# Performance work log

Hardware: AMD Instinct MI355X
Metric: run time of the kernel (lower is better)

The kernel has to match this reference:

```python
import jax, jax.numpy as jnp
import numpy as np

N, E, C = 50000, 600000, 128
BN_EPS = 1e-5
NORM_EPS = 1e-12


def _edgeconv(x, src, dst, wa, ba, g, be, rm, rv, wb, bb):
    # PyG EdgeConv: message = MLP(concat(x_i, x_j - x_i)); aggr='add' at target i
    x_i = x[dst]                      # [E, C] target features
    x_j = x[src]                      # [E, C] source features
    m = jnp.concatenate([x_i, x_j - x_i], axis=-1)   # [E, 2C]
    m = jax.nn.relu(m @ wa.T + ba)                   # Linear(2C->C) + ReLU
    m = (m - rm) * (g * jax.lax.rsqrt(rv + BN_EPS)) + be  # BatchNorm1d (eval)
    m = m @ wb.T + bb                                # Linear(C->C)
    return jax.ops.segment_sum(m, dst, num_segments=x.shape[0])  # [N, C]


def _lin(k, fan_in, shape):
    bound = 1.0 / np.sqrt(fan_in)
    return jax.random.uniform(k, shape, jnp.float32, -bound, bound)


def setup_inputs() -> dict:
    key = jax.random.key(0)
    ks = jax.random.split(key, 16)
    inp = {
        "x": jax.random.normal(ks[0], (N, C), jnp.float32),
        "edge_index": jax.random.randint(ks[1], (2, E), 0, N, jnp.int64),
    }
    # layer 1 params
    inp["w1a"] = _lin(ks[2], 2 * C, (C, 2 * C)); inp["b1a"] = _lin(ks[3], 2 * C, (C,))
    inp["g1"] = jnp.ones((C,), jnp.float32) + 0.1 * jax.random.normal(ks[4], (C,))
    inp["be1"] = 0.1 * jax.random.normal(ks[5], (C,))
    inp["rm1"] = 0.1 * jax.random.normal(ks[6], (C,))
    inp["rv1"] = 0.5 + jax.random.uniform(ks[7], (C,))
    inp["w1b"] = _lin(ks[8], C, (C, C)); inp["b1b"] = _lin(ks[9], C, (C,))
    # layer 2 params
    inp["w2a"] = _lin(ks[10], 2 * C, (C, 2 * C)); inp["b2a"] = _lin(ks[11], 2 * C, (C,))
    inp["g2"] = jnp.ones((C,), jnp.float32) + 0.1 * jax.random.normal(ks[12], (C,))
    inp["be2"] = 0.1 * jax.random.normal(ks[13], (C,))
    inp["rm2"] = 0.1 * jax.random.normal(ks[14], (C,))
    inp["rv2"] = 0.5 + jax.random.uniform(ks[15], (C,))
    k2 = jax.random.split(ks[15], 2)
    inp["w2b"] = _lin(k2[0], C, (C, C)); inp["b2b"] = _lin(k2[1], C, (C,))
    return inp


def reference(x, edge_index, w1a, b1a, g1, be1, rm1, rv1, w1b, b1b,
              w2a, b2a, g2, be2, rm2, rv2, w2b, b2b):
    src, dst = edge_index[0], edge_index[1]
    # layer 1 (all but last): conv -> relu -> L2 normalize -> dropout(eval=identity)
    h = _edgeconv(x, src, dst, w1a, b1a, g1, be1, rm1, rv1, w1b, b1b)
    h = jax.nn.relu(h)
    h = h / jnp.maximum(jnp.linalg.norm(h, axis=-1, keepdims=True), NORM_EPS)
    # last layer: conv only
    return _edgeconv(h, src, dst, w2a, b2a, g2, be2, rm2, rv2, w2b, b2b)
```

## Files before the change

kernel.cpp:

```cpp
#include <hip/hip_runtime.h>

#define CCH 128
#define WPAD 136
typedef unsigned short ushort;
typedef __attribute__((ext_vector_type(8))) short bf16x8_t;
typedef __attribute__((ext_vector_type(4))) float f32x4;

union ABu { bf16x8_t v; ushort u[8]; uint4 q; };

__device__ __forceinline__ ushort f2b(float f) {
  union { float f; unsigned u; } v{f};
  unsigned r = v.u + 0x7fffu + ((v.u >> 16) & 1u);
  return (ushort)(r >> 16);
}
__device__ __forceinline__ float b2f(ushort s) {
  union { unsigned u; float f; } v{(unsigned)s << 16};
  return v.f;
}

__global__ void k_detect(const unsigned int* __restrict__ eiw, int* __restrict__ flags) {
  __shared__ int cz;
  int t = threadIdx.x;
  if (t == 0) cz = 0;
  __syncthreads();
  if (eiw[2 * t + 1] != 0u) atomicAdd(&cz, 1);
  __syncthreads();
  if (t == 0) flags[1] = (cz == 0) ? 1 : 0;
}

__device__ __forceinline__ int ldidx(const void* ei, size_t i, bool i64) {
  return i64 ? (int)((const long long*)ei)[i] : ((const int*)ei)[i];
}

__global__ void k_hist(const void* __restrict__ ei, int* __restrict__ deg, int E,
                       const int* __restrict__ flags) {
  bool i64 = flags[1] != 0;
  int e = blockIdx.x * 256 + threadIdx.x;
  if (e < E) atomicAdd(&deg[ldidx(ei, (size_t)E + e, i64)], 1);
}

__global__ void k_scan1(const int* __restrict__ deg, int* __restrict__ bsum, int n) {
  __shared__ int s[256];
  int t = threadIdx.x, i = blockIdx.x * 256 + t;
  s[t] = (i < n) ? deg[i] : 0;
  __syncthreads();
  for (int off = 128; off > 0; off >>= 1) {
    if (t < off) s[t] += s[t + off];
    __syncthreads();
  }
  if (t == 0) bsum[blockIdx.x] = s[0];
}

__global__ void k_scan2(const int* __restrict__ bsum, int* __restrict__ boff, int nb) {
  __shared__ int s[256];
  int t = threadIdx.x;
  int v = (t < nb) ? bsum[t] : 0;
  s[t] = v; __syncthreads();
  for (int off = 1; off < 256; off <<= 1) {
    int tv = (t >= off) ? s[t - off] : 0;
    __syncthreads();
    s[t] += tv;
    __syncthreads();
  }
  if (t < nb) boff[t] = s[t] - v;
}

__global__ void k_scan3(const int* __restrict__ deg, const int* __restrict__ boff,
                        int* __restrict__ rowptr, int n, int Etot) {
  __shared__ int s[256];
  int t = threadIdx.x, i = blockIdx.x * 256 + t;
  int v = (i < n) ? deg[i] : 0;
  s[t] = v; __syncthreads();
  for (int off = 1; off < 256; off <<= 1) {
    int tv = (t >= off) ? s[t - off] : 0;
    __syncthreads();
    s[t] += tv;
    __syncthreads();
  }
  if (i < n) rowptr[i] = boff[blockIdx.x] + s[t] - v;
  if (i == 0) rowptr[n] = Etot;
}

__global__ void k_scatter(const void* __restrict__ ei, const int* __restrict__ rowptr,
                          int* __restrict__ cnt, int* __restrict__ esrc, int E,
                          const int* __restrict__ flags) {
  bool i64 = flags[1] != 0;
  int e = blockIdx.x * 256 + threadIdx.x;
  if (e < E) {
    int d = ldidx(ei, (size_t)E + e, i64);
    int s = ldidx(ei, (size_t)e, i64);
    int pos = rowptr[d] + atomicAdd(&cnt[d], 1);
    esrc[pos] = s;
  }
}

__global__ void k_wconv(const float* __restrict__ wa, const float* __restrict__ wb,
                        ushort* __restrict__ Wcat, ushort* __restrict__ Wbb) {
  int i = blockIdx.x * 256 + threadIdx.x;
  if (i < 32768) {
    int c = i >> 7, k = i & 127;
    float v = (c < 128) ? wa[c * 256 + k] - wa[c * 256 + 128 + k]
                        : wa[(c - 128) * 256 + 128 + k];
    Wcat[i] = f2b(v);
  }
  if (i < 16384) Wbb[i] = f2b(wb[i]);
}

template <int EPI, typename TIN>
__global__ __launch_bounds__(256) void k_gemm(const TIN* __restrict__ X,
                                              const ushort* __restrict__ W,
                                              const float* __restrict__ bias,
                                              const int* __restrict__ deg,
                                              void* __restrict__ Y1,
                                              ushort* __restrict__ Y2, int nN) {
  constexpr int WN = (EPI == 0) ? 16 : 8;
  __shared__ ushort wlds[WN * 16 * WPAD];
  const int t = threadIdx.x;
  const int wave = t >> 6, lane = t & 63;
  const int ln = lane & 15, quad = lane >> 4;

  for (int i = t; i < WN * 256; i += 256) {
    int row = i >> 4, ch = i & 15;
    *(uint4*)&wlds[row * WPAD + ch * 8] = *(const uint4*)&W[row * CCH + ch * 8];
  }
  __syncthreads();

  const int rowb0 = blockIdx.x * 128 + wave * 32;
  const int rowb1 = rowb0 + 16;
  const int ar0 = rowb0 + ln, ar1 = rowb1 + ln;

  ABu a0[4], a1[4];
#pragma unroll
  for (int kk = 0; kk < 4; ++kk) {
    if constexpr (sizeof(TIN) == 4) {
      auto ldc = [&](int r, ABu& d) {
        if (r < nN) {
          const float* xp = (const float*)X + (size_t)r * CCH + kk * 32 + quad * 8;
          float4 f0 = *(const float4*)xp;
          float4 f1 = *(const float4*)(xp + 4);
          d.u[0] = f2b(f0.x); d.u[1] = f2b(f0.y); d.u[2] = f2b(f0.z); d.u[3] = f2b(f0.w);
          d.u[4] = f2b(f1.x); d.u[5] = f2b(f1.y); d.u[6] = f2b(f1.z); d.u[7] = f2b(f1.w);
        } else d.q = make_uint4(0, 0, 0, 0);
      };
      ldc(ar0, a0[kk]); ldc(ar1, a1[kk]);
    } else {
      a0[kk].q = (ar0 < nN) ? *(const uint4*)((const ushort*)X + (size_t)ar0 * CCH + kk * 32 + quad * 8)
                            : make_uint4(0, 0, 0, 0);
      a1[kk].q = (ar1 < nN) ? *(const uint4*)((const ushort*)X + (size_t)ar1 * CCH + kk * 32 + quad * 8)
                            : make_uint4(0, 0, 0, 0);
    }
  }

  f32x4 acc0[WN], acc1[WN];
#pragma unroll
  for (int s = 0; s < WN; ++s) {
    acc0[s] = (f32x4){0.f, 0.f, 0.f, 0.f};
    acc1[s] = (f32x4){0.f, 0.f, 0.f, 0.f};
  }

#pragma unroll
  for (int s = 0; s < WN; ++s) {
#pragma unroll
    for (int kk = 0; kk < 4; ++kk) {
      ABu b;
      b.q = *(const uint4*)&wlds[(s * 16 + ln) * WPAD + kk * 32 + quad * 8];
      acc0[s] = __builtin_amdgcn_mfma_f32_16x16x32_bf16(a0[kk].v, b.v, acc0[s], 0, 0, 0);
      acc1[s] = __builtin_amdgcn_mfma_f32_16x16x32_bf16(a1[kk].v, b.v, acc1[s], 0, 0, 0);
    }
  }

  if constexpr (EPI == 0) {
    ushort* A1 = (ushort*)Y1;
#pragma unroll
    for (int s = 0; s < 16; ++s) {
      int col = s * 16 + ln;
      float bv = (s < 8) ? bias[col] : 0.f;
#pragma unroll
      for (int r = 0; r < 4; ++r) {
        int row0 = rowb0 + quad * 4 + r, row1 = rowb1 + quad * 4 + r;
        if (row0 < nN) {
          if (s < 8) A1[(size_t)row0 * CCH + col] = f2b(acc0[s][r] + bv);
          else       Y2[(size_t)row0 * CCH + (col - 128)] = f2b(acc0[s][r]);
        }
        if (row1 < nN) {
          if (s < 8) A1[(size_t)row1 * CCH + col] = f2b(acc1[s][r] + bv);
          else       Y2[(size_t)row1 * CCH + (col - 128)] = f2b(acc1[s][r]);
        }
      }
    }
  } else if constexpr (EPI == 1) {
    ushort* H = (ushort*)Y1;
    float biasv[8];
#pragma unroll
    for (int s = 0; s < 8; ++s) biasv[s] = bias[s * 16 + ln];
    auto epi = [&](f32x4* acc, int rowb) {
#pragma unroll
      for (int r = 0; r < 4; ++r) {
        int row = rowb + quad * 4 + r;
        float dn = (row < nN) ? (float)deg[row] : 0.f;
        float vals[8];
        float ss = 0.f;
#pragma unroll
        for (int s = 0; s < 8; ++s) {
          float v = fmaxf(acc[s][r] + dn * biasv[s], 0.f);
          vals[s] = v;
          ss += v * v;
        }
        ss += __shfl_xor(ss, 1, 64);
        ss += __shfl_xor(ss, 2, 64);
        ss += __shfl_xor(ss, 4, 64);
        ss += __shfl_xor(ss, 8, 64);
        float inv = 1.0f / fmaxf(sqrtf(ss), 1e-12f);
        if (row < nN) {
#pragma unroll
          for (int s = 0; s < 8; ++s)
            H[(size_t)row * CCH + s * 16 + ln] = f2b(vals[s] * inv);
        }
      }
    };
    epi(acc0, rowb0); epi(acc1, rowb1);
  } else {
    float* OUT = (float*)Y1;
    float biasv[8];
#pragma unroll
    for (int s = 0; s < 8; ++s) biasv[s] = bias[s * 16 + ln];
    auto epi = [&](f32x4* acc, int rowb) {
#pragma unroll
      for (int r = 0; r < 4; ++r) {
        int row = rowb + quad * 4 + r;
        if (row >= nN) continue;
        float dn = (float)deg[row];
#pragma unroll
        for (int s = 0; s < 8; ++s)
          OUT[(size_t)row * CCH + s * 16 + ln] = acc[s][r] + dn * biasv[s];
      }
    };
    epi(acc0, rowb0); epi(acc1, rowb1);
  }
}

__global__ __launch_bounds__(256) void k_aggr(const ushort* __restrict__ A1,
                                              const ushort* __restrict__ A2,
                                              const int* __restrict__ rowptr,
                                              const int* __restrict__ esrc,
                                              const float* __restrict__ g,
                                              const float* __restrict__ be,
                                              const float* __restrict__ rm,
                                              const float* __restrict__ rv,
                                              ushort* __restrict__ M, int nNodes) {
  int node = blockIdx.x * 4 + (threadIdx.x >> 6);
  if (node >= nNodes) return;
  int lane = threadIdx.x & 63;
  int q = lane >> 4;
  int c = (lane & 15) * 8;

  uint4 aq = *(const uint4*)&A1[(size_t)node * CCH + c];
  float a[8] = {b2f((ushort)aq.x), b2f((ushort)(aq.x >> 16)),
                b2f((ushort)aq.y), b2f((ushort)(aq.y >> 16)),
                b2f((ushort)aq.z), b2f((ushort)(aq.z >> 16)),
                b2f((ushort)aq.w), b2f((ushort)(aq.w >> 16))};
  int r0 = rowptr[node], r1 = rowptr[node + 1];
  float s[8] = {0.f, 0.f, 0.f, 0.f, 0.f, 0.f, 0.f, 0.f};

  int e = r0 + q;
  for (; e + 4 < r1; e += 8) {
    int sA = esrc[e], sB = esrc[e + 4];
    uint4 wA = *(const uint4*)&A2[(size_t)sA * CCH + c];
    uint4 wB = *(const uint4*)&A2[(size_t)sB * CCH + c];
    const unsigned* pA = (const unsigned*)&wA;
    const unsigned* pB = (const unsigned*)&wB;
#pragma unroll
    for (int j = 0; j < 4; ++j) {
      s[2*j]   += fmaxf(a[2*j]   + b2f((ushort)pA[j]), 0.f);
      s[2*j+1] += fmaxf(a[2*j+1] + b2f((ushort)(pA[j] >> 16)), 0.f);
      s[2*j]   += fmaxf(a[2*j]   + b2f((ushort)pB[j]), 0.f);
      s[2*j+1] += fmaxf(a[2*j+1] + b2f((ushort)(pB[j] >> 16)), 0.f);
    }
  }
  for (; e < r1; e += 4) {
    int sA = esrc[e];
    uint4 wA = *(const uint4*)&A2[(size_t)sA * CCH + c];
    const unsigned* pA = (const unsigned*)&wA;
#pragma unroll
    for (int j = 0; j < 4; ++j) {
      s[2*j]   += fmaxf(a[2*j]   + b2f((ushort)pA[j]), 0.f);
      s[2*j+1] += fmaxf(a[2*j+1] + b2f((ushort)(pA[j] >> 16)), 0.f);
    }
  }
#pragma unroll
  for (int j = 0; j < 8; ++j) {
    s[j] += __shfl_xor(s[j], 16, 64);
    s[j] += __shfl_xor(s[j], 32, 64);
  }

  if (q == 0) {
    float dn = (float)(r1 - r0);
    unsigned p[4];
#pragma unroll
    for (int j = 0; j < 4; ++j) {
      float sc0 = g[c + 2*j]     * rsqrtf(rv[c + 2*j]     + 1e-5f);
      float sc1 = g[c + 2*j + 1] * rsqrtf(rv[c + 2*j + 1] + 1e-5f);
      float o0 = sc0 * s[2*j]     + dn * (be[c + 2*j]     - rm[c + 2*j]     * sc0);
      float o1 = sc1 * s[2*j + 1] + dn * (be[c + 2*j + 1] - rm[c + 2*j + 1] * sc1);
      p[j] = (unsigned)f2b(o0) | ((unsigned)f2b(o1) << 16);
    }
    *(uint4*)&M[(size_t)node * CCH + c] = make_uint4(p[0], p[1], p[2], p[3]);
  }
}

extern "C" void kernel_launch(void* const* d_in, const int* in_sizes, int n_in,
                              void* d_out, int out_size, void* d_ws, size_t ws_size,
                              hipStream_t stream) {
  const float* x   = (const float*)d_in[0];
  const void*  ei  = d_in[1];
  const float* w1a = (const float*)d_in[2];
  const float* b1a = (const float*)d_in[3];
  const float* g1  = (const float*)d_in[4];
  const float* be1 = (const float*)d_in[5];
  const float* rm1 = (const float*)d_in[6];
  const float* rv1 = (const float*)d_in[7];
  const float* w1b = (const float*)d_in[8];
  const float* b1b = (const float*)d_in[9];
  const float* w2a = (const float*)d_in[10];
  const float* b2a = (const float*)d_in[11];
  const float* g2  = (const float*)d_in[12];
  const float* be2 = (const float*)d_in[13];
  const float* rm2 = (const float*)d_in[14];
  const float* rv2 = (const float*)d_in[15];
  const float* w2b = (const float*)d_in[16];
  const float* b2b = (const float*)d_in[17];

  const int N = in_sizes[0] / CCH;
  const int E = in_sizes[1] / 2;
  const size_t NC = (size_t)N * CCH;

  int* flags  = (int*)d_ws;
  int* deg    = flags + 4;
  int* cnt    = deg + N;
  int* rowptr = cnt + N;
  int* bsum   = rowptr + N + 1;
  int* boff   = bsum + 256;
  int* esrc   = boff + 256;
  uintptr_t pw = ((uintptr_t)(esrc + E) + 63) & ~(uintptr_t)63;
  ushort* Wcat1 = (ushort*)pw;
  ushort* Wcat2 = Wcat1 + 32768;
  ushort* Wb1   = Wcat2 + 32768;
  ushort* Wb2   = Wb1 + 16384;
  uintptr_t pb = ((uintptr_t)(Wb2 + 16384) + 63) & ~(uintptr_t)63;
  ushort* B0 = (ushort*)pb;
  ushort* B1 = B0 + NC;
  ushort* MB = B1 + NC;
  ushort* HB = MB + NC;

  const int gE = (E + 255) / 256;
  const int gS = (N + 255) / 256;
  const int gG = (N + 127) / 128;
  const int gA = (N + 3) / 4;

  k_detect<<<1, 256, 0, stream>>>((const unsigned int*)ei, flags);
  hipMemsetAsync(deg, 0, sizeof(int) * 2 * (size_t)N, stream);
  k_wconv<<<128, 256, 0, stream>>>(w1a, w1b, Wcat1, Wb1);
  k_wconv<<<128, 256, 0, stream>>>(w2a, w2b, Wcat2, Wb2);
  k_hist<<<gE, 256, 0, stream>>>(ei, deg, E, flags);
  k_scan1<<<gS, 256, 0, stream>>>(deg, bsum, N);
  k_scan2<<<1, 256, 0, stream>>>(bsum, boff, gS);
  k_scan3<<<gS, 256, 0, stream>>>(deg, boff, rowptr, N, E);
  k_scatter<<<gE, 256, 0, stream>>>(ei, rowptr, cnt, esrc, E, flags);

  k_gemm<0, float><<<gG, 256, 0, stream>>>(x, Wcat1, b1a, nullptr, B0, B1, N);
  k_aggr<<<gA, 256, 0, stream>>>(B0, B1, rowptr, esrc, g1, be1, rm1, rv1, MB, N);
  k_gemm<1, ushort><<<gG, 256, 0, stream>>>(MB, Wb1, b1b, deg, HB, nullptr, N);
  k_gemm<0, ushort><<<gG, 256, 0, stream>>>(HB, Wcat2, b2a, nullptr, B0, B1, N);
  k_aggr<<<gA, 256, 0, stream>>>(B0, B1, rowptr, esrc, g2, be2, rm2, rv2, MB, N);
  k_gemm<2, ushort><<<gG, 256, 0, stream>>>(MB, Wb2, b2b, deg, d_out, nullptr, N);
}
```

Before: 313.4 us.

## Fuse setup kernels and shrink GEMM tiles with a column-split grid

```diff
diff --git a/kernel.cpp b/kernel.cpp
--- a/kernel.cpp
+++ b/kernel.cpp
@@ -18,18 +18,42 @@
   return v.f;
 }
 
-__global__ void k_detect(const unsigned int* __restrict__ eiw, int* __restrict__ flags) {
-  __shared__ int cz;
-  int t = threadIdx.x;
-  if (t == 0) cz = 0;
-  __syncthreads();
-  if (eiw[2 * t + 1] != 0u) atomicAdd(&cz, 1);
-  __syncthreads();
-  if (t == 0) flags[1] = (cz == 0) ? 1 : 0;
-}
-
 __device__ __forceinline__ int ldidx(const void* ei, size_t i, bool i64) {
   return i64 ? (int)((const long long*)ei)[i] : ((const int*)ei)[i];
+}
+
+__global__ void k_init(const unsigned int* __restrict__ eiw, int* __restrict__ flags,
+                       int* __restrict__ degcnt, int n2,
+                       const float* __restrict__ w1a, const float* __restrict__ w1b,
+                       const float* __restrict__ w2a, const float* __restrict__ w2b,
+                       ushort* __restrict__ Wcat1, ushort* __restrict__ Wb1,
+                       ushort* __restrict__ Wcat2, ushort* __restrict__ Wb2) {
+  int b = blockIdx.x, t = threadIdx.x;
+  int gid = b * 256 + t;
+  if (gid < n2) degcnt[gid] = 0;
+
+  if (b < 128) {
+    int i = gid;
+    int c = i >> 7, k = i & 127;
+    float v = (c < 128) ? w1a[c * 256 + k] - w1a[c * 256 + 128 + k]
+                        : w1a[(c - 128) * 256 + 128 + k];
+    Wcat1[i] = f2b(v);
+    if (i < 16384) Wb1[i] = f2b(w1b[i]);
+  } else if (b < 256) {
+    int i = gid - 32768;
+    int c = i >> 7, k = i & 127;
+    float v = (c < 128) ? w2a[c * 256 + k] - w2a[c * 256 + 128 + k]
+                        : w2a[(c - 128) * 256 + 128 + k];
+    Wcat2[i] = f2b(v);
+    if (i < 16384) Wb2[i] = f2b(w2b[i]);
+  } else if (b == 256) {
+    __shared__ int cz;
+    if (t == 0) cz = 0;
+    __syncthreads();
+    if (eiw[2 * t + 1] != 0u) atomicAdd(&cz, 1);
+    __syncthreads();
+    if (t == 0) flags[1] = (cz == 0) ? 1 : 0;
+  }
 }
 
 __global__ void k_hist(const void* __restrict__ ei, int* __restrict__ deg, int E,
@@ -94,18 +118,6 @@
   }
 }
 
-__global__ void k_wconv(const float* __restrict__ wa, const float* __restrict__ wb,
-                        ushort* __restrict__ Wcat, ushort* __restrict__ Wbb) {
-  int i = blockIdx.x * 256 + threadIdx.x;
-  if (i < 32768) {
-    int c = i >> 7, k = i & 127;
-    float v = (c < 128) ? wa[c * 256 + k] - wa[c * 256 + 128 + k]
-                        : wa[(c - 128) * 256 + 128 + k];
-    Wcat[i] = f2b(v);
-  }
-  if (i < 16384) Wbb[i] = f2b(wb[i]);
-}
-
 template <int EPI, typename TIN>
 __global__ __launch_bounds__(256) void k_gemm(const TIN* __restrict__ X,
                                               const ushort* __restrict__ W,
@@ -113,79 +125,63 @@
                                               const int* __restrict__ deg,
                                               void* __restrict__ Y1,
                                               ushort* __restrict__ Y2, int nN) {
-  constexpr int WN = (EPI == 0) ? 16 : 8;
-  __shared__ ushort wlds[WN * 16 * WPAD];
+  __shared__ ushort wlds[128 * WPAD];
   const int t = threadIdx.x;
   const int wave = t >> 6, lane = t & 63;
   const int ln = lane & 15, quad = lane >> 4;
-
-  for (int i = t; i < WN * 256; i += 256) {
+  const int half = (EPI == 0) ? blockIdx.y : 0;
+
+  const ushort* Wp = W + (size_t)half * 128 * CCH;
+  for (int i = t; i < 128 * 16; i += 256) {
     int row = i >> 4, ch = i & 15;
-    *(uint4*)&wlds[row * WPAD + ch * 8] = *(const uint4*)&W[row * CCH + ch * 8];
+    *(uint4*)&wlds[row * WPAD + ch * 8] = *(const uint4*)&Wp[row * CCH + ch * 8];
   }
   __syncthreads();
 
-  const int rowb0 = blockIdx.x * 128 + wave * 32;
-  const int rowb1 = rowb0 + 16;
-  const int ar0 = rowb0 + ln, ar1 = rowb1 + ln;
-
-  ABu a0[4], a1[4];
+  const int rowb = blockIdx.x * 64 + wave * 16;
+  const int arow = rowb + ln;
+
+  ABu a[4];
 #pragma unroll
   for (int kk = 0; kk < 4; ++kk) {
     if constexpr (sizeof(TIN) == 4) {
-      auto ldc = [&](int r, ABu& d) {
-        if (r < nN) {
-          const float* xp = (const float*)X + (size_t)r * CCH + kk * 32 + quad * 8;
-          float4 f0 = *(const float4*)xp;
-          float4 f1 = *(const float4*)(xp + 4);
-          d.u[0] = f2b(f0.x); d.u[1] = f2b(f0.y); d.u[2] = f2b(f0.z); d.u[3] = f2b(f0.w);
-          d.u[4] = f2b(f1.x); d.u[5] = f2b(f1.y); d.u[6] = f2b(f1.z); d.u[7] = f2b(f1.w);
-        } else d.q = make_uint4(0, 0, 0, 0);
-      };
-      ldc(ar0, a0[kk]); ldc(ar1, a1[kk]);
+      if (arow < nN) {
+        const float* xp = (const float*)X + (size_t)arow * CCH + kk * 32 + quad * 8;
+        float4 f0 = *(const float4*)xp;
+        float4 f1 = *(const float4*)(xp + 4);
+        a[kk].u[0] = f2b(f0.x); a[kk].u[1] = f2b(f0.y); a[kk].u[2] = f2b(f0.z); a[kk].u[3] = f2b(f0.w);
+        a[kk].u[4] = f2b(f1.x); a[kk].u[5] = f2b(f1.y); a[kk].u[6] = f2b(f1.z); a[kk].u[7] = f2b(f1.w);
+      } else a[kk].q = make_uint4(0, 0, 0, 0);
     } else {
-      a0[kk].q = (ar0 < nN) ? *(const uint4*)((const ushort*)X + (size_t)ar0 * CCH + kk * 32 + quad * 8)
+      a[kk].q = (arow < nN) ? *(const uint4*)((const ushort*)X + (size_t)arow * CCH + kk * 32 + quad * 8)
                             : make_uint4(0, 0, 0, 0);
-      a1[kk].q = (ar1 < nN) ? *(const uint4*)((const ushort*)X + (size_t)ar1 * CCH + kk * 32 + quad * 8)
-                            : make_uint4(0, 0, 0, 0);
-    }
-  }
-
-  f32x4 acc0[WN], acc1[WN];
-#pragma unroll
-  for (int s = 0; s < WN; ++s) {
-    acc0[s] = (f32x4){0.f, 0.f, 0.f, 0.f};
-    acc1[s] = (f32x4){0.f, 0.f, 0.f, 0.f};
-  }
-
-#pragma unroll
-  for (int s = 0; s < WN; ++s) {
+    }
+  }
+
+  f32x4 acc[8];
+#pragma unroll
+  for (int s = 0; s < 8; ++s) acc[s] = (f32x4){0.f, 0.f, 0.f, 0.f};
+
+#pragma unroll
+  for (int s = 0; s < 8; ++s) {
 #pragma unroll
     for (int kk = 0; kk < 4; ++kk) {
       ABu b;
       b.q = *(const uint4*)&wlds[(s * 16 + ln) * WPAD + kk * 32 + quad * 8];
-      acc0[s] = __builtin_amdgcn_mfma_f32_16x16x32_bf16(a0[kk].v, b.v, acc0[s], 0, 0, 0);
-      acc1[s] = __builtin_amdgcn_mfma_f32_16x16x32_bf16(a1[kk].v, b.v, acc1[s], 0, 0, 0);
+      acc[s] = __builtin_amdgcn_mfma_f32_16x16x32_bf16(a[kk].v, b.v, acc[s], 0, 0, 0);
     }
   }
 
   if constexpr (EPI == 0) {
-    ushort* A1 = (ushort*)Y1;
-#pragma unroll
-    for (int s = 0; s < 16; ++s) {
+    ushort* dst = half ? Y2 : (ushort*)Y1;
+#pragma unroll
+    for (int s = 0; s < 8; ++s) {
       int col = s * 16 + ln;
-      float bv = (s < 8) ? bias[col] : 0.f;
+      float bv = half ? 0.f : bias[col];
 #pragma unroll
       for (int r = 0; r < 4; ++r) {
-        int row0 = rowb0 + quad * 4 + r, row1 = rowb1 + quad * 4 + r;
-        if (row0 < nN) {
-          if (s < 8) A1[(size_t)row0 * CCH + col] = f2b(acc0[s][r] + bv);
-          else       Y2[(size_t)row0 * CCH + (col - 128)] = f2b(acc0[s][r]);
-        }
-        if (row1 < nN) {
-          if (s < 8) A1[(size_t)row1 * CCH + col] = f2b(acc1[s][r] + bv);
-          else       Y2[(size_t)row1 * CCH + (col - 128)] = f2b(acc1[s][r]);
-        }
+        int row = rowb + quad * 4 + r;
+        if (row < nN) dst[(size_t)row * CCH + col] = f2b(acc[s][r] + bv);
       }
     }
   } else if constexpr (EPI == 1) {
@@ -193,49 +189,43 @@
     float biasv[8];
 #pragma unroll
     for (int s = 0; s < 8; ++s) biasv[s] = bias[s * 16 + ln];
-    auto epi = [&](f32x4* acc, int rowb) {
-#pragma unroll
-      for (int r = 0; r < 4; ++r) {
-        int row = rowb + quad * 4 + r;
-        float dn = (row < nN) ? (float)deg[row] : 0.f;
-        float vals[8];
-        float ss = 0.f;
-#pragma unroll
-        for (int s = 0; s < 8; ++s) {
-          float v = fmaxf(acc[s][r] + dn * biasv[s], 0.f);
-          vals[s] = v;
-          ss += v * v;
-        }
-        ss += __shfl_xor(ss, 1, 64);
-        ss += __shfl_xor(ss, 2, 64);
-        ss += __shfl_xor(ss, 4, 64);
-        ss += __shfl_xor(ss, 8, 64);
-        float inv = 1.0f / fmaxf(sqrtf(ss), 1e-12f);
-        if (row < nN) {
-#pragma unroll
-          for (int s = 0; s < 8; ++s)
-            H[(size_t)row * CCH + s * 16 + ln] = f2b(vals[s] * inv);
-        }
+#pragma unroll
+    for (int r = 0; r < 4; ++r) {
+      int row = rowb + quad * 4 + r;
+      float dn = (row < nN) ? (float)deg[row] : 0.f;
+      float vals[8];
+      float ss = 0.f;
+#pragma unroll
+      for (int s = 0; s < 8; ++s) {
+        float v = fmaxf(acc[s][r] + dn * biasv[s], 0.f);
+        vals[s] = v;
+        ss += v * v;
       }
-    };
-    epi(acc0, rowb0); epi(acc1, rowb1);
+      ss += __shfl_xor(ss, 1, 64);
+      ss += __shfl_xor(ss, 2, 64);
+      ss += __shfl_xor(ss, 4, 64);
+      ss += __shfl_xor(ss, 8, 64);
+      float inv = 1.0f / fmaxf(sqrtf(ss), 1e-12f);
+      if (row < nN) {
+#pragma unroll
+        for (int s = 0; s < 8; ++s)
+          H[(size_t)row * CCH + s * 16 + ln] = f2b(vals[s] * inv);
+      }
+    }
   } else {
     float* OUT = (float*)Y1;
     float biasv[8];
 #pragma unroll
     for (int s = 0; s < 8; ++s) biasv[s] = bias[s * 16 + ln];
-    auto epi = [&](f32x4* acc, int rowb) {
-#pragma unroll
-      for (int r = 0; r < 4; ++r) {
-        int row = rowb + quad * 4 + r;
-        if (row >= nN) continue;
-        float dn = (float)deg[row];
-#pragma unroll
-        for (int s = 0; s < 8; ++s)
-          OUT[(size_t)row * CCH + s * 16 + ln] = acc[s][r] + dn * biasv[s];
-      }
-    };
-    epi(acc0, rowb0); epi(acc1, rowb1);
+#pragma unroll
+    for (int r = 0; r < 4; ++r) {
+      int row = rowb + quad * 4 + r;
+      if (row >= nN) continue;
+      float dn = (float)deg[row];
+#pragma unroll
+      for (int s = 0; s < 8; ++s)
+        OUT[(size_t)row * CCH + s * 16 + ln] = acc[s][r] + dn * biasv[s];
+    }
   }
 }
 
@@ -354,23 +344,23 @@
 
   const int gE = (E + 255) / 256;
   const int gS = (N + 255) / 256;
-  const int gG = (N + 127) / 128;
+  const int gG = (N + 63) / 64;
   const int gA = (N + 3) / 4;
-
-  k_detect<<<1, 256, 0, stream>>>((const unsigned int*)ei, flags);
-  hipMemsetAsync(deg, 0, sizeof(int) * 2 * (size_t)N, stream);
-  k_wconv<<<128, 256, 0, stream>>>(w1a, w1b, Wcat1, Wb1);
-  k_wconv<<<128, 256, 0, stream>>>(w2a, w2b, Wcat2, Wb2);
+  int gInit = (2 * N + 255) / 256;
+  if (gInit < 257) gInit = 257;
+
+  k_init<<<gInit, 256, 0, stream>>>((const unsigned int*)ei, flags, deg, 2 * N,
+                                    w1a, w1b, w2a, w2b, Wcat1, Wb1, Wcat2, Wb2);
   k_hist<<<gE, 256, 0, stream>>>(ei, deg, E, flags);
   k_scan1<<<gS, 256, 0, stream>>>(deg, bsum, N);
   k_scan2<<<1, 256, 0, stream>>>(bsum, boff, gS);
   k_scan3<<<gS, 256, 0, stream>>>(deg, boff, rowptr, N, E);
   k_scatter<<<gE, 256, 0, stream>>>(ei, rowptr, cnt, esrc, E, flags);
 
-  k_gemm<0, float><<<gG, 256, 0, stream>>>(x, Wcat1, b1a, nullptr, B0, B1, N);
+  k_gemm<0, float><<<dim3(gG, 2), 256, 0, stream>>>(x, Wcat1, b1a, deg, B0, B1, N);
   k_aggr<<<gA, 256, 0, stream>>>(B0, B1, rowptr, esrc, g1, be1, rm1, rv1, MB, N);
   k_gemm<1, ushort><<<gG, 256, 0, stream>>>(MB, Wb1, b1b, deg, HB, nullptr, N);
-  k_gemm<0, ushort><<<gG, 256, 0, stream>>>(HB, Wcat2, b2a, nullptr, B0, B1, N);
+  k_gemm<0, ushort><<<dim3(gG, 2), 256, 0, stream>>>(HB, Wcat2, b2a, deg, B0, B1, N);
   k_aggr<<<gA, 256, 0, stream>>>(B0, B1, rowptr, esrc, g2, be2, rm2, rv2, MB, N);
   k_gemm<2, ushort><<<gG, 256, 0, stream>>>(MB, Wb2, b2b, deg, d_out, nullptr, N);
 }
```

Measured after the change: 300.8 us. 4.0% less time.
